# Kernel tuning notes

Hardware: AMD Instinct MI355X
Metric: run time of the kernel (lower is better)

Reference implementation:

```python
import jax, jax.numpy as jnp
import numpy as np

HEADS = 4
HEAD_DIM = 128  # GATConv out_channels
NEG_SLOPE_ATT = 0.2   # GATConv internal leaky relu
NEG_SLOPE_ACT = 0.01  # nn.LeakyReLU() default


def gat_conv(x, edge_index, W, att_src, att_dst, bias):
    # x: [N, F]; edge_index: [2, E] (row 0 = src j, row 1 = dst i)
    N = x.shape[0]
    h = (x @ W).reshape(N, HEADS, HEAD_DIM)            # [N, H, C]
    loops = jnp.arange(N, dtype=edge_index.dtype)
    src = jnp.concatenate([edge_index[0], loops])      # add self loops
    dst = jnp.concatenate([edge_index[1], loops])
    a_src = jnp.einsum('nhc,hc->nh', h, att_src)       # [N, H]
    a_dst = jnp.einsum('nhc,hc->nh', h, att_dst)
    e = jax.nn.leaky_relu(a_src[src] + a_dst[dst], NEG_SLOPE_ATT)  # [E', H]
    # segment softmax over incoming edges of each dst node
    emax = jax.ops.segment_max(e, dst, num_segments=N)
    ex = jnp.exp(e - emax[dst])
    denom = jax.ops.segment_sum(ex, dst, num_segments=N)
    alpha = ex / (denom[dst] + 1e-16)                  # [E', H]
    msg = h[src] * alpha[:, :, None]                   # [E', H, C]
    out = jax.ops.segment_sum(msg, dst, num_segments=N)
    return out.reshape(N, HEADS * HEAD_DIM) + bias     # [N, H*C]


def branch(x, edge_index, W, att_src, att_dst, bias, fc1_w, fc1_b):
    h = gat_conv(x, edge_index, W, att_src, att_dst, bias)
    h = jax.nn.leaky_relu(h, NEG_SLOPE_ACT)
    g = jnp.mean(h, axis=0, keepdims=True)             # global mean pool, batch all zeros -> [1, H*C]
    g = jax.nn.leaky_relu(g @ fc1_w + fc1_b, NEG_SLOPE_ACT)
    return g  # dropout is identity in eval mode


def setup_inputs() -> dict:
    key = jax.random.key(0)
    ks = jax.random.split(key, 10)
    N, E, F = 20000, 320000, 512
    HC = HEADS * HEAD_DIM
    s = 1.0 / np.sqrt(F)
    return {
        'x': jax.random.normal(ks[0], (N, F), jnp.float32),
        'adj': jax.random.randint(ks[1], (2, E), 0, N, jnp.int64),
        'wt_x': jax.random.normal(ks[2], (N, F), jnp.float32),
        'wt_adj': jax.random.randint(ks[3], (2, E), 0, N, jnp.int64),
        'W': jax.random.normal(ks[4], (F, HC), jnp.float32) * s,
        'att_src': jax.random.normal(ks[5], (HEADS, HEAD_DIM), jnp.float32) * s,
        'att_dst': jax.random.normal(ks[6], (HEADS, HEAD_DIM), jnp.float32) * s,
        'bias': jnp.zeros((HC,), jnp.float32),
        'fc1_w': jax.random.normal(ks[7], (HC, 512), jnp.float32) * (1.0 / np.sqrt(HC)),
        'fc1_b': jnp.zeros((512,), jnp.float32),
    }


def reference(x, adj, wt_x, wt_adj, W, att_src, att_dst, bias, fc1_w, fc1_b):
    g = branch(x, adj, W, att_src, att_dst, bias, fc1_w, fc1_b)
    wt_g = branch(wt_x, wt_adj, W, att_src, att_dst, bias, fc1_w, fc1_b)
    xd = g - wt_g
    return jnp.concatenate([g, wt_g, xd], axis=1)  # [1, 3*512]
```

## Files before the change

### kernel.cpp

```cpp
#include <hip/hip_runtime.h>
#include <hip/hip_bf16.h>

typedef unsigned short u16;
typedef short bf16x8 __attribute__((ext_vector_type(8)));
typedef float f32x4 __attribute__((ext_vector_type(4)));
typedef float f32x2 __attribute__((ext_vector_type(2)));

__device__ __forceinline__ u16 f2b(float f) {
    unsigned x = __float_as_uint(f);
    return (u16)((x + 0x7fffu + ((x >> 16) & 1u)) >> 16);
}

__device__ __forceinline__ int pkbf(float lo, float hi) {
    return __builtin_amdgcn_perm(__float_as_uint(hi), __float_as_uint(lo), 0x07060302);
}

__global__ void cast_wt_kernel(const float* __restrict__ W, u16* __restrict__ Wt) {
    int idx = blockIdx.x * blockDim.x + threadIdx.x;
    int n = idx >> 9, k = idx & 511;
    Wt[idx] = f2b(W[k * 512 + n]);
}

__global__ __launch_bounds__(256, 2) void gemm_fused2(
    const float* __restrict__ xA, const float* __restrict__ xW, const u16* __restrict__ Bt,
    unsigned char* __restrict__ h8, const float* __restrict__ att_src,
    const float* __restrict__ att_dst, float* __restrict__ asrc, float* __restrict__ adst,
    int N, int Mpad) {
    __shared__ float lA[128 * 32];
    __shared__ u16 lB[128 * 32];
    __shared__ float sred[2][128][2];
    const int tid = threadIdx.x;
    const int w = tid >> 6, l = tid & 63;
    const int row0 = blockIdx.y * 128;
    const int head = blockIdx.x;
    const int col0 = head * 128;
    const int wr = w >> 1, wc = w & 1;
    const int mlane = l & 15, quad = l >> 4;
    const int R2v = 2 * Mpad;

    const float* src = (row0 >= Mpad) ? xW : xA;
    const int rbase = row0 - (row0 >= Mpad ? Mpad : 0);
    const int arow = (w << 3) + (l >> 3);
    const int acol = (l & 7) << 2;
    const int srow = (w << 4) + (l >> 2);
    const int scol = (l & 3) << 3;

    f32x4 acc[4][4];
#pragma unroll
    for (int i = 0; i < 4; i++)
#pragma unroll
        for (int j = 0; j < 4; j++) acc[i][j] = f32x4{0.f, 0.f, 0.f, 0.f};

    for (int k0 = 0; k0 < 512; k0 += 32) {
#pragma unroll
        for (int g = 0; g < 4; ++g) {
            int lrow = rbase + g * 32 + arow;
            lrow = min(lrow, N - 1);
            const float* ga = src + (size_t)lrow * 512 + k0 + acol;
            float* la = lA + (g * 32 + (w << 3)) * 32;
            __builtin_amdgcn_global_load_lds((const __attribute__((address_space(1))) void*)ga,
                                             (__attribute__((address_space(3))) void*)la, 16, 0, 0);
        }
#pragma unroll
        for (int s = 0; s < 2; ++s) {
            const u16* gb = Bt + (size_t)(col0 + s * 64 + srow) * 512 + (k0 + scol);
            u16* lb = lB + s * 2048 + w * 512;
            __builtin_amdgcn_global_load_lds((const __attribute__((address_space(1))) void*)gb,
                                             (__attribute__((address_space(3))) void*)lb, 16, 0, 0);
        }
        __syncthreads();
        bf16x8 af[4], bfr[4];
#pragma unroll
        for (int i = 0; i < 4; i++) {
            const float* ap = &lA[(wr * 64 + i * 16 + mlane) * 32 + quad * 8];
            float4 f0 = *(const float4*)ap;
            float4 f1 = *(const float4*)(ap + 4);
            int* ai = (int*)&af[i];
            ai[0] = pkbf(f0.x, f0.y);
            ai[1] = pkbf(f0.z, f0.w);
            ai[2] = pkbf(f1.x, f1.y);
            ai[3] = pkbf(f1.z, f1.w);
            bfr[i] = *(const bf16x8*)&lB[(wc * 64 + i * 16 + mlane) * 32 + quad * 8];
        }
#pragma unroll
        for (int i = 0; i < 4; i++)
#pragma unroll
            for (int j = 0; j < 4; j++)
                acc[i][j] = __builtin_amdgcn_mfma_f32_16x16x32_bf16(af[i], bfr[j], acc[i][j], 0, 0, 0);
        __syncthreads();
    }

    float as_j[4], ad_j[4];
#pragma unroll
    for (int j = 0; j < 4; j++) {
        as_j[j] = att_src[col0 + wc * 64 + j * 16 + mlane];
        ad_j[j] = att_dst[col0 + wc * 64 + j * 16 + mlane];
    }
#pragma unroll
    for (int i = 0; i < 4; i++) {
#pragma unroll
        for (int r = 0; r < 4; r++) {
            float vs = 0.f, vd = 0.f;
#pragma unroll
            for (int j = 0; j < 4; j++) {
                float hv = acc[i][j][r];
                vs += hv * as_j[j];
                vd += hv * ad_j[j];
            }
#pragma unroll
            for (int o = 8; o >= 1; o >>= 1) {
                vs += __shfl_xor(vs, o);
                vd += __shfl_xor(vd, o);
            }
            if (mlane == 0) {
                int lrow = wr * 64 + i * 16 + quad * 4 + r;
                sred[0][lrow][wc] = vs;
                sred[1][lrow][wc] = vd;
            }
        }
    }
#pragma unroll
    for (int i = 0; i < 4; i++)
#pragma unroll
        for (int j = 0; j < 4; j++)
#pragma unroll
            for (int r = 0; r < 4; r++) {
                int rg = row0 + wr * 64 + i * 16 + quad * 4 + r;
                int cc = wc * 64 + j * 16 + mlane;
                float v = acc[i][j][r];
                unsigned pk = __builtin_amdgcn_cvt_pk_fp8_f32(v, v, 0, false);
                h8[(((size_t)(head * R2v + rg)) << 7) + cc] = (unsigned char)(pk & 0xff);
            }
    __syncthreads();
    {
        int row = tid & 127, which = tid >> 7;
        int rg = row0 + row;
        float v = sred[which][row][0] + sred[which][row][1];
        (which ? adst : asrc)[head * R2v + rg] = v;
    }
}

__global__ void csr_count(const int* __restrict__ adj, const int* __restrict__ wadj,
                          int E, int Mpad, int* __restrict__ deg) {
    int i = blockIdx.x * blockDim.x + threadIdx.x;
    if (i < 2 * E) {
        int d = (i < E) ? adj[E + i] : (wadj[E + (i - E)] + Mpad);
        atomicAdd(&deg[d], 1);
    }
}

__global__ __launch_bounds__(256) void scanA(const int* __restrict__ deg, int* __restrict__ off,
                                             int* __restrict__ bsum, int n, int N, int Mpad) {
    __shared__ int wsum[4];
    int tid = threadIdx.x, lane = tid & 63, wid = tid >> 6;
    int i = blockIdx.x * 256 + tid;
    int valid = (i < N) || (i >= Mpad && i < Mpad + N);
    int d = (i < n) ? deg[i] + (valid ? 1 : 0) : 0;
    int x = d;
#pragma unroll
    for (int o = 1; o < 64; o <<= 1) {
        int y = __shfl_up(x, (unsigned)o, 64);
        if (lane >= o) x += y;
    }
    if (lane == 63) wsum[wid] = x;
    __syncthreads();
    int woff = 0;
    for (int j = 0; j < wid; ++j) woff += wsum[j];
    if (i < n) off[i] = woff + x - d;
    if (tid == 255) bsum[blockIdx.x] = woff + x;
}

__global__ __launch_bounds__(256) void scanB(const int* __restrict__ bsum, int* __restrict__ bbase,
                                             int nb, int* __restrict__ off, int n) {
    __shared__ int wsum[4];
    int tid = threadIdx.x, lane = tid & 63, wid = tid >> 6;
    int d = (tid < nb) ? bsum[tid] : 0;
    int x = d;
#pragma unroll
    for (int o = 1; o < 64; o <<= 1) {
        int y = __shfl_up(x, (unsigned)o, 64);
        if (lane >= o) x += y;
    }
    if (lane == 63) wsum[wid] = x;
    __syncthreads();
    int woff = 0;
    for (int j = 0; j < wid; ++j) woff += wsum[j];
    int excl = woff + x - d;
    if (tid < nb) bbase[tid] = excl;
    if (tid == nb - 1) off[n] = excl + d;
}

__global__ void scanC(int* __restrict__ off, const int* __restrict__ bbase,
                      int* __restrict__ cursor, int* __restrict__ csrc, int n, int N, int Mpad) {
    int i = blockIdx.x * blockDim.x + threadIdx.x;
    if (i < n) {
        int o = off[i] + bbase[i >> 8];
        off[i] = o;
        int valid = (i < N) || (i >= Mpad && i < Mpad + N);
        if (valid) csrc[o] = i;
        cursor[i] = o + valid;
    }
}

__global__ void csr_scatter(const int* __restrict__ adj, const int* __restrict__ wadj,
                            int E, int Mpad, int* __restrict__ cursor, int* __restrict__ csrc) {
    int i = blockIdx.x * blockDim.x + threadIdx.x;
    if (i < 2 * E) {
        int s, d;
        if (i < E) {
            s = adj[i];
            d = adj[E + i];
        } else {
            s = wadj[i - E] + Mpad;
            d = wadj[E + (i - E)] + Mpad;
        }
        int p = atomicAdd(&cursor[d], 1);
        csrc[p] = s;
    }
}

__device__ __forceinline__ void edgeH(int hr, bool valid, float ad,
                                      const float* __restrict__ ash,
                                      const unsigned char* __restrict__ h8h, int ch,
                                      float* acc, float& dsum) {
    float e = ash[hr] + ad;
    e = fmaxf(e, 0.2f * e);
    float ex = __expf(e);
    ex = valid ? ex : 0.f;
    dsum += ex;
    int2 hv = *(const int2*)(h8h + (((size_t)hr) << 7) + ch);
    f32x2 f01 = __builtin_amdgcn_cvt_pk_f32_fp8(hv.x, false);
    f32x2 f23 = __builtin_amdgcn_cvt_pk_f32_fp8(hv.x, true);
    f32x2 f45 = __builtin_amdgcn_cvt_pk_f32_fp8(hv.y, false);
    f32x2 f67 = __builtin_amdgcn_cvt_pk_f32_fp8(hv.y, true);
    acc[0] += ex * f01.x; acc[1] += ex * f01.y;
    acc[2] += ex * f23.x; acc[3] += ex * f23.y;
    acc[4] += ex * f45.x; acc[5] += ex * f45.y;
    acc[6] += ex * f67.x; acc[7] += ex * f67.y;
}

__global__ __launch_bounds__(256) void gat_aggregate8(
    const unsigned char* __restrict__ h8, const float* __restrict__ asrc,
    const float* __restrict__ adst, const int* __restrict__ off, const int* __restrict__ csrc,
    const float* __restrict__ bias, float* __restrict__ partAB, int Mpad) {
    const int R2 = 2 * Mpad;
    __shared__ float spool[256];
    int tid = threadIdx.x;
    spool[tid] = 0.f;
    __syncthreads();
    int wv = tid >> 6, l = tid & 63;
    int g = l >> 4;
    int ch = (l & 15) << 3;
    int head = (blockIdx.x & 7) >> 1;
    const unsigned char* h8h = h8 + (((size_t)head * R2) << 7);
    const float* ash = asrc + (size_t)head * R2;
    const float* adh = adst + (size_t)head * R2;
    float bb[8];
#pragma unroll
    for (int k = 0; k < 8; ++k) bb[k] = bias[head * 128 + ch + k];
    float poolA[8] = {0.f, 0.f, 0.f, 0.f, 0.f, 0.f, 0.f, 0.f};
    float poolB[8] = {0.f, 0.f, 0.f, 0.f, 0.f, 0.f, 0.f, 0.f};

    int widx = ((((blockIdx.x >> 3) << 1) | (blockIdx.x & 1)) << 2) + wv;
    const int stride = gridDim.x;
    for (int d = widx; d < R2; d += stride) {
        int qa = off[d];
        int n = off[d + 1] - qa;
        float ad = adh[d];
        float acc[8] = {0.f, 0.f, 0.f, 0.f, 0.f, 0.f, 0.f, 0.f};
        float dsum = 0.f;
        for (int base = 0; base < n; base += 8) {
            int i0 = base + (g << 1);
            bool v0 = i0 < n, v1 = i0 + 1 < n;
            int e0 = csrc[qa + (v0 ? i0 : 0)];
            int e1 = csrc[qa + (v1 ? i0 + 1 : 0)];
            edgeH(e0, v0, ad, ash, h8h, ch, acc, dsum);
            edgeH(e1, v1, ad, ash, h8h, ch, acc, dsum);
        }
        dsum += __shfl_xor(dsum, 16);
        dsum += __shfl_xor(dsum, 32);
#pragma unroll
        for (int k = 0; k < 8; ++k) {
            acc[k] += __shfl_xor(acc[k], 16);
            acc[k] += __shfl_xor(acc[k], 32);
        }
        if (n > 0) {
            float inv = 1.f / (dsum + 1e-16f);
            if (d >= Mpad) {
#pragma unroll
                for (int k = 0; k < 8; ++k) {
                    float o = acc[k] * inv + bb[k];
                    poolB[k] += fmaxf(o, 0.01f * o);
                }
            } else {
#pragma unroll
                for (int k = 0; k < 8; ++k) {
                    float o = acc[k] * inv + bb[k];
                    poolA[k] += fmaxf(o, 0.01f * o);
                }
            }
        }
    }
    if (l < 16) {
#pragma unroll
        for (int k = 0; k < 8; ++k) {
            atomicAdd(&spool[ch + k], poolA[k]);
            atomicAdd(&spool[128 + ch + k], poolB[k]);
        }
    }
    __syncthreads();
    {
        int base = (blockIdx.x & 63) << 9;
        int c = tid & 127;
        float v = spool[tid];
        float* dp = (tid < 128) ? (partAB + base + head * 128 + c)
                                : (partAB + 64 * 512 + base + head * 128 + c);
        atomicAdd(dp, v);
    }
}

__global__ __launch_bounds__(256) void fc_final2(
    const float* __restrict__ partAB, const float* __restrict__ w, const float* __restrict__ b,
    float* __restrict__ out, float invN) {
    __shared__ float gA[512], gB[512];
    __shared__ float rA[256], rB[256];
    int t = threadIdx.x;
    for (int i = t; i < 512; i += 256) {
        float sA = 0.f, sB = 0.f;
        for (int r = 0; r < 64; ++r) {
            sA += partAB[r * 512 + i];
            sB += partAB[64 * 512 + r * 512 + i];
        }
        gA[i] = sA * invN;
        gB[i] = sB * invN;
    }
    __syncthreads();
    int jj = t & 31, ks = t >> 5;
    int j = blockIdx.x * 32 + jj;
    float sA = 0.f, sB = 0.f;
    for (int k = ks * 64; k < ks * 64 + 64; ++k) {
        float wv = w[k * 512 + j];
        sA += gA[k] * wv;
        sB += gB[k] * wv;
    }
    rA[t] = sA;
    rB[t] = sB;
    __syncthreads();
    if (ks == 0) {
#pragma unroll
        for (int s2 = 1; s2 < 8; ++s2) {
            sA += rA[jj + 32 * s2];
            sB += rB[jj + 32 * s2];
        }
        sA += b[j];
        sB += b[j];
        sA = sA >= 0.f ? sA : 0.01f * sA;
        sB = sB >= 0.f ? sB : 0.01f * sB;
        out[j] = sA;
        out[512 + j] = sB;
        out[1024 + j] = sA - sB;
    }
}

extern "C" void kernel_launch(void* const* d_in, const int* in_sizes, int n_in,
                              void* d_out, int out_size, void* d_ws, size_t ws_size,
                              hipStream_t stream) {
    const float* x = (const float*)d_in[0];
    const int* adj = (const int*)d_in[1];
    const float* wtx = (const float*)d_in[2];
    const int* wadj = (const int*)d_in[3];
    const float* W = (const float*)d_in[4];
    const float* att_s = (const float*)d_in[5];
    const float* att_d = (const float*)d_in[6];
    const float* bias = (const float*)d_in[7];
    const float* fc1w = (const float*)d_in[8];
    const float* fc1b = (const float*)d_in[9];
    float* out = (float*)d_out;

    const int N = in_sizes[0] / 512;
    const int E = in_sizes[1] / 2;
    const int Mpad = ((N + 127) / 128) * 128;
    const int R2 = 2 * Mpad;
    const int nb = (R2 + 255) / 256;

    char* p = (char*)d_ws;
    auto alloc = [&](size_t bytes) -> char* {
        char* r = p;
        p += (bytes + 255) & ~(size_t)255;
        return r;
    };
    unsigned char* h8 = (unsigned char*)alloc((size_t)R2 * 512);
    u16* Wt = (u16*)alloc(512 * 512 * 2);
    float* asrc = (float*)alloc((size_t)R2 * 4 * 4);
    float* adst = (float*)alloc((size_t)R2 * 4 * 4);
    int* deg = (int*)alloc((size_t)R2 * 4);
    int* off = (int*)alloc((size_t)(R2 + 1) * 4);
    int* cursor = (int*)alloc((size_t)R2 * 4);
    int* bsum = (int*)alloc(256 * 4);
    int* bbase = (int*)alloc(256 * 4);
    int* csrc = (int*)alloc((size_t)2 * (E + N) * 4);
    float* partAB = (float*)alloc((size_t)2 * 64 * 512 * 4);

    hipMemsetAsync(partAB, 0, (size_t)2 * 64 * 512 * 4, stream);
    hipMemsetAsync(deg, 0, (size_t)R2 * 4, stream);
    cast_wt_kernel<<<(512 * 512) / 256, 256, 0, stream>>>(W, Wt);

    csr_count<<<(2 * E + 255) / 256, 256, 0, stream>>>(adj, wadj, E, Mpad, deg);
    scanA<<<nb, 256, 0, stream>>>(deg, off, bsum, R2, N, Mpad);
    scanB<<<1, 256, 0, stream>>>(bsum, bbase, nb, off, R2);
    scanC<<<nb, 256, 0, stream>>>(off, bbase, cursor, csrc, R2, N, Mpad);
    csr_scatter<<<(2 * E + 255) / 256, 256, 0, stream>>>(adj, wadj, E, Mpad, cursor, csrc);

    dim3 gg(4, R2 / 128, 1);
    gemm_fused2<<<gg, 256, 0, stream>>>(x, wtx, Wt, h8, att_s, att_d, asrc, adst, N, Mpad);

    gat_aggregate8<<<2048, 256, 0, stream>>>(h8, asrc, adst, off, csrc, bias, partAB, Mpad);

    fc_final2<<<16, 256, 0, stream>>>(partAB, fc1w, fc1b, out, 1.0f / (float)N);
}
```

Baseline: 366.4 us.

## Restructure GAT aggregation: two dst nodes per wave, 16B loads, software prefetch

The aggregation kernel now processes two destination nodes per wavefront, one per half-wave, with each lane handling 16 channels through 16-byte fp8 loads instead of 8. The edge loop is software-pipelined so the next edge's source index, attention logit and feature row load while the current edge is accumulated. Accumulation uses packed v_pk_fma_f32 through inline asm. The aim is more memory-level parallelism and fewer instructions per edge. The cost is divergence when the paired nodes have unequal degrees, and clamped extra loads.

```diff
diff --git a/kernel.cpp b/kernel.cpp
--- a/kernel.cpp
+++ b/kernel.cpp
@@ -13,6 +13,10 @@
 
 __device__ __forceinline__ int pkbf(float lo, float hi) {
     return __builtin_amdgcn_perm(__float_as_uint(hi), __float_as_uint(lo), 0x07060302);
+}
+
+__device__ __forceinline__ void pkfma(f32x2& acc, f32x2 f, f32x2 ex) {
+    asm("v_pk_fma_f32 %0, %1, %2, %0" : "+v"(acc) : "v"(f), "v"(ex));
 }
 
 __global__ void cast_wt_kernel(const float* __restrict__ W, u16* __restrict__ Wt) {
@@ -219,94 +223,102 @@
     }
 }
 
-__device__ __forceinline__ void edgeH(int hr, bool valid, float ad,
-                                      const float* __restrict__ ash,
-                                      const unsigned char* __restrict__ h8h, int ch,
-                                      float* acc, float& dsum) {
-    float e = ash[hr] + ad;
-    e = fmaxf(e, 0.2f * e);
-    float ex = __expf(e);
-    ex = valid ? ex : 0.f;
-    dsum += ex;
-    int2 hv = *(const int2*)(h8h + (((size_t)hr) << 7) + ch);
-    f32x2 f01 = __builtin_amdgcn_cvt_pk_f32_fp8(hv.x, false);
-    f32x2 f23 = __builtin_amdgcn_cvt_pk_f32_fp8(hv.x, true);
-    f32x2 f45 = __builtin_amdgcn_cvt_pk_f32_fp8(hv.y, false);
-    f32x2 f67 = __builtin_amdgcn_cvt_pk_f32_fp8(hv.y, true);
-    acc[0] += ex * f01.x; acc[1] += ex * f01.y;
-    acc[2] += ex * f23.x; acc[3] += ex * f23.y;
-    acc[4] += ex * f45.x; acc[5] += ex * f45.y;
-    acc[6] += ex * f67.x; acc[7] += ex * f67.y;
-}
-
-__global__ __launch_bounds__(256) void gat_aggregate8(
+__global__ __launch_bounds__(256) void gat_aggregate9(
     const unsigned char* __restrict__ h8, const float* __restrict__ asrc,
     const float* __restrict__ adst, const int* __restrict__ off, const int* __restrict__ csrc,
-    const float* __restrict__ bias, float* __restrict__ partAB, int Mpad) {
+    const float* __restrict__ bias, float* __restrict__ partAB, int Mpad, int Em1) {
     const int R2 = 2 * Mpad;
     __shared__ float spool[256];
     int tid = threadIdx.x;
     spool[tid] = 0.f;
     __syncthreads();
-    int wv = tid >> 6, l = tid & 63;
-    int g = l >> 4;
-    int ch = (l & 15) << 3;
-    int head = (blockIdx.x & 7) >> 1;
+    const int wv = tid >> 6, l = tid & 63;
+    const int gi = (l >> 3) & 3;
+    const int hi = l >> 5;
+    const int chb = (l & 7) << 4;
+    const int head = (blockIdx.x & 7) >> 1;
     const unsigned char* h8h = h8 + (((size_t)head * R2) << 7);
     const float* ash = asrc + (size_t)head * R2;
     const float* adh = adst + (size_t)head * R2;
-    float bb[8];
-#pragma unroll
-    for (int k = 0; k < 8; ++k) bb[k] = bias[head * 128 + ch + k];
-    float poolA[8] = {0.f, 0.f, 0.f, 0.f, 0.f, 0.f, 0.f, 0.f};
-    float poolB[8] = {0.f, 0.f, 0.f, 0.f, 0.f, 0.f, 0.f, 0.f};
+    float bb[16];
+#pragma unroll
+    for (int k = 0; k < 16; ++k) bb[k] = bias[head * 128 + chb + k];
+    float pool[16];
+#pragma unroll
+    for (int k = 0; k < 16; ++k) pool[k] = 0.f;
 
     int widx = ((((blockIdx.x >> 3) << 1) | (blockIdx.x & 1)) << 2) + wv;
-    const int stride = gridDim.x;
-    for (int d = widx; d < R2; d += stride) {
-        int qa = off[d];
-        int n = off[d + 1] - qa;
-        float ad = adh[d];
-        float acc[8] = {0.f, 0.f, 0.f, 0.f, 0.f, 0.f, 0.f, 0.f};
+    int hf = widx >> 10;
+    int aw = widx & 1023;
+    const int hb = hf * Mpad;
+    const int half = Mpad >> 1;
+
+    for (int p = aw; p < half; p += 1024) {
+        int d0 = (p << 1) + hb;
+        int q0 = off[d0], q1 = off[d0 + 1], q2 = off[d0 + 2];
+        int n0 = q1 - q0, n1 = q2 - q1;
+        int nmax = max(n0, n1);
+        if (nmax == 0) continue;
+        int nm = hi ? n1 : n0;
+        int qm = hi ? q1 : q0;
+        float ad = adh[d0 + hi];
+        f32x2 acc2[8];
+#pragma unroll
+        for (int j = 0; j < 8; ++j) acc2[j] = f32x2{0.f, 0.f};
         float dsum = 0.f;
-        for (int base = 0; base < n; base += 8) {
-            int i0 = base + (g << 1);
-            bool v0 = i0 < n, v1 = i0 + 1 < n;
-            int e0 = csrc[qa + (v0 ? i0 : 0)];
-            int e1 = csrc[qa + (v1 ? i0 + 1 : 0)];
-            edgeH(e0, v0, ad, ash, h8h, ch, acc, dsum);
-            edgeH(e1, v1, ad, ash, h8h, ch, acc, dsum);
-        }
+
+        int i0 = gi;
+        int e0 = csrc[min(qm + ((i0 < nm) ? i0 : 0), Em1)];
+        float acur = ash[e0];
+        int4 hcur = *(const int4*)(h8h + (((size_t)e0) << 7) + chb);
+        int i1 = 4 + gi;
+        int enext = csrc[min(qm + ((i1 < nm) ? i1 : 0), Em1)];
+
+        for (int base = 0; base < nmax; base += 4) {
+            float anext = ash[enext];
+            int4 hnext = *(const int4*)(h8h + (((size_t)enext) << 7) + chb);
+            int i2 = base + 8 + gi;
+            int e2 = csrc[min(qm + ((i2 < nm) ? i2 : 0), Em1)];
+            float e = acur + ad;
+            float em = fmaxf(e, 0.2f * e);
+            float ex = __expf(em);
+            ex = ((base + gi) < nm) ? ex : 0.f;
+            dsum += ex;
+            f32x2 exv = {ex, ex};
+            f32x2 f;
+            f = __builtin_amdgcn_cvt_pk_f32_fp8(hcur.x, false); pkfma(acc2[0], f, exv);
+            f = __builtin_amdgcn_cvt_pk_f32_fp8(hcur.x, true);  pkfma(acc2[1], f, exv);
+            f = __builtin_amdgcn_cvt_pk_f32_fp8(hcur.y, false); pkfma(acc2[2], f, exv);
+            f = __builtin_amdgcn_cvt_pk_f32_fp8(hcur.y, true);  pkfma(acc2[3], f, exv);
+            f = __builtin_amdgcn_cvt_pk_f32_fp8(hcur.z, false); pkfma(acc2[4], f, exv);
+            f = __builtin_amdgcn_cvt_pk_f32_fp8(hcur.z, true);  pkfma(acc2[5], f, exv);
+            f = __builtin_amdgcn_cvt_pk_f32_fp8(hcur.w, false); pkfma(acc2[6], f, exv);
+            f = __builtin_amdgcn_cvt_pk_f32_fp8(hcur.w, true);  pkfma(acc2[7], f, exv);
+            acur = anext; hcur = hnext; enext = e2;
+        }
+        dsum += __shfl_xor(dsum, 8);
         dsum += __shfl_xor(dsum, 16);
-        dsum += __shfl_xor(dsum, 32);
-#pragma unroll
-        for (int k = 0; k < 8; ++k) {
-            acc[k] += __shfl_xor(acc[k], 16);
-            acc[k] += __shfl_xor(acc[k], 32);
-        }
-        if (n > 0) {
+#pragma unroll
+        for (int j = 0; j < 8; ++j) {
+            acc2[j].x += __shfl_xor(acc2[j].x, 8);
+            acc2[j].y += __shfl_xor(acc2[j].y, 8);
+            acc2[j].x += __shfl_xor(acc2[j].x, 16);
+            acc2[j].y += __shfl_xor(acc2[j].y, 16);
+        }
+        if (nm > 0) {
             float inv = 1.f / (dsum + 1e-16f);
-            if (d >= Mpad) {
-#pragma unroll
-                for (int k = 0; k < 8; ++k) {
-                    float o = acc[k] * inv + bb[k];
-                    poolB[k] += fmaxf(o, 0.01f * o);
-                }
-            } else {
-#pragma unroll
-                for (int k = 0; k < 8; ++k) {
-                    float o = acc[k] * inv + bb[k];
-                    poolA[k] += fmaxf(o, 0.01f * o);
-                }
+#pragma unroll
+            for (int j = 0; j < 8; ++j) {
+                float o0 = acc2[j].x * inv + bb[2 * j];
+                float o1 = acc2[j].y * inv + bb[2 * j + 1];
+                pool[2 * j] += fmaxf(o0, 0.01f * o0);
+                pool[2 * j + 1] += fmaxf(o1, 0.01f * o1);
             }
         }
     }
-    if (l < 16) {
-#pragma unroll
-        for (int k = 0; k < 8; ++k) {
-            atomicAdd(&spool[ch + k], poolA[k]);
-            atomicAdd(&spool[128 + ch + k], poolB[k]);
-        }
+    if ((l & 31) < 8) {
+#pragma unroll
+        for (int k = 0; k < 16; ++k) atomicAdd(&spool[hf * 128 + chb + k], pool[k]);
     }
     __syncthreads();
     {
@@ -414,7 +426,8 @@
     dim3 gg(4, R2 / 128, 1);
     gemm_fused2<<<gg, 256, 0, stream>>>(x, wtx, Wt, h8, att_s, att_d, asrc, adst, N, Mpad);
 
-    gat_aggregate8<<<2048, 256, 0, stream>>>(h8, asrc, adst, off, csrc, bias, partAB, Mpad);
+    gat_aggregate9<<<2048, 256, 0, stream>>>(h8, asrc, adst, off, csrc, bias, partAB, Mpad,
+                                             2 * (E + N) - 1);
 
     fc_final2<<<16, 256, 0, stream>>>(partAB, fc1w, fc1b, out, 1.0f / (float)N);
 }
```

After: 349.0 us. -4.7%, faster.
